# Optimization experiments

Hardware: AMD Instinct MI355X
Metric: run time of the kernel (lower is better)

## Reference

```python
import jax, jax.numpy as jnp
from jax import lax
import numpy as np

B, N, E, NA = 32, 8192, 256, 16
M_MIN, M_MAX = 3, 8192
PAD_TOKEN = -2.0
LN_EPS = 1e-3  # keras LayerNormalization default epsilon


def setup_inputs() -> dict:
    key = jax.random.key(0)
    ks = jax.random.split(key, 8)
    return {
        "x": jax.random.normal(ks[0], (B, N, E), jnp.float32),
        "mask": jnp.ones((B, N), jnp.float32),
        "barcode": jax.random.uniform(ks[1], (1, 1, E), jnp.float32),
        "Wq": 0.05 * jax.random.normal(ks[2], (E, E), jnp.float32),
        "Wk": 0.05 * jax.random.normal(ks[3], (E, E), jnp.float32),
        "Wv": 0.05 * jax.random.normal(ks[4], (E, E), jnp.float32),
        "g": jax.random.uniform(ks[5], (NA, E, E), jnp.float32, minval=-0.05, maxval=0.05),
        "w": 0.05 * jax.random.normal(ks[6], (1, NA, E, E), jnp.float32),
        "ln_gamma": jnp.ones((E,), jnp.float32),
        "ln_beta": jnp.zeros((E,), jnp.float32),
    }


def _select_one(order):
    """Greedy distance-constrained selection over a descending-sorted index list (N,).
    Matches the TF while_loop: first index always kept; a candidate is kept iff its
    abs distance to every previously kept index lies in [M_MIN, M_MAX].
    Unfilled slots stay 0 (TensorArray default)."""
    slot = jnp.arange(NA, dtype=jnp.int32)

    def body(i, state):
        sel, count = state
        cand = order[i]
        d = jnp.abs(sel - cand)
        ok = (d >= M_MIN) & (d <= M_MAX)
        active = slot < count
        valid = jnp.all(jnp.where(active, ok, True)) & (count < NA)
        sel = jnp.where((slot == count) & valid, cand, sel)
        count = count + valid.astype(jnp.int32)
        return (sel, count)

    sel0 = jnp.zeros((NA,), jnp.int32).at[0].set(order[0])
    sel, _ = lax.fori_loop(1, N, body, (sel0, jnp.int32(1)))
    return sel


def reference(x, mask, barcode, Wq, Wk, Wv, g, w, ln_gamma, ln_beta):
    m = jnp.where(mask == PAD_TOKEN, 0.0, 1.0)  # (B, N)
    bc = jnp.broadcast_to(barcode, (x.shape[0], 1, x.shape[-1]))
    q = bc @ Wq              # (B, 1, E)
    k = x @ Wk               # (B, N, E)
    v = x @ Wv               # (B, N, E)
    scale = 1.0 / jnp.sqrt(jnp.float32(x.shape[-1]))
    att = jnp.einsum('bqe,bne->bqn', q, k) * scale  # (B, 1, N)
    att = att + (1.0 - m[:, None, :]) * (-1e9)
    att = jax.nn.softmax(att, axis=-1) * m[:, None, :]
    barcode_out = jnp.einsum('bqn,bne->bqe', att, v)[:, 0, :]  # (B, E)

    att1 = att[:, 0, :]                                 # (B, N)
    order = jnp.argsort(-att1, axis=-1).astype(jnp.int32)
    inds = jnp.sort(jax.vmap(_select_one)(order), axis=-1)  # (B, NA)
    weights = jnp.take_along_axis(att1, inds, axis=1)        # (B, NA)
    outs = jnp.take_along_axis(x, inds[:, :, None], axis=1)  # (B, NA, E)

    # sinusoidal positional encoding from anchor positions
    ra = jnp.arange(E, dtype=jnp.float32) / jnp.float32(E)
    pos = jnp.sin(inds[:, :, None].astype(jnp.float32) / jnp.power(40.0, ra))
    outs = outs + pos

    # per-anchor gated projection: (B,NA,1,E) @ (NA,E,E) -> (B,NA,E)
    outs_w = jnp.einsum('bae,aef->baf', outs, w[0])
    outs_g = jax.nn.sigmoid(jnp.einsum('bae,aef->baf', outs, g))
    outs = outs_w * outs_g * weights[:, :, None]

    # LayerNorm over last axis (keras defaults: eps=1e-3, learned gamma/beta)
    mu = jnp.mean(outs, axis=-1, keepdims=True)
    var = jnp.mean(jnp.square(outs - mu), axis=-1, keepdims=True)
    outs = (outs - mu) * lax.rsqrt(var + LN_EPS) * ln_gamma + ln_beta

    return (outs, inds, weights, barcode_out)
```

## Files before the change

kernel.cpp:

```cpp
#include <hip/hip_runtime.h>

#define BB 32
#define NN 8192
#define EE 256
#define NAA 16
#define NCHUNK 64
#define CHUNK 128

#define KQ_OFF   0
#define ATT_OFF  256
#define PL_OFF   (ATT_OFF + BB*NN)
#define PS_OFF   (PL_OFF + BB*NCHUNK)
#define INDS_OFF (PS_OFF + BB*NCHUNK*EE)
#define WSEL_OFF (INDS_OFF + BB*NAA)

#define OUT_OUTS 0
#define OUT_INDS (BB*NAA*EE)
#define OUT_W    (OUT_INDS + BB*NAA)
#define OUT_BC   (OUT_W + BB*NAA)

__global__ __launch_bounds__(1024) void prep_kernel(
    const float* __restrict__ barcode, const float* __restrict__ Wq,
    const float* __restrict__ Wk, float* __restrict__ ws) {
  int t = threadIdx.x & 255, q = threadIdx.x >> 8;
  __shared__ float part[4][EE];
  __shared__ float qs[EE];
  float acc = 0.f;
  #pragma unroll 8
  for (int i = 0; i < 64; ++i) {
    int f = q * 64 + i;
    acc += barcode[f] * Wq[f*EE + t];
  }
  part[q][t] = acc;
  __syncthreads();
  if (threadIdx.x < 256) qs[t] = part[0][t] + part[1][t] + part[2][t] + part[3][t];
  __syncthreads();
  const float4* wk4 = (const float4*)(Wk + (size_t)t * EE + q * 64);
  const float4* qs4 = (const float4*)(qs + q * 64);
  float acc2 = 0.f;
  #pragma unroll
  for (int i = 0; i < 16; ++i) {
    float4 wv = wk4[i], qv = qs4[i];
    acc2 += wv.x*qv.x + wv.y*qv.y + wv.z*qv.z + wv.w*qv.w;
  }
  part[q][t] = acc2;
  __syncthreads();
  if (threadIdx.x < 256)
    ws[KQ_OFF + t] = (part[0][t] + part[1][t] + part[2][t] + part[3][t]) * 0.0625f;
}

__global__ __launch_bounds__(256) void pass_a(
    const float* __restrict__ x, const float* __restrict__ mask,
    float* __restrict__ ws) {
  const int c = blockIdx.x, b = blockIdx.y;
  const int w = threadIdx.x >> 6, lane = threadIdx.x & 63;
  const float4 kq4 = ((const float4*)(ws + KQ_OFF))[lane];
  float* att = ws + ATT_OFF + (size_t)b * NN + c * CHUNK;
  const float* xb = x + ((size_t)b * NN + (size_t)c * CHUNK) * EE;
  const float* mb = mask + (size_t)b * NN + c * CHUNK;

  float l = 0.f;
  float4 acc = {0.f, 0.f, 0.f, 0.f};
  #pragma unroll 4
  for (int r = w; r < CHUNK; r += 4) {
    float4 xv = ((const float4*)(xb + (size_t)r * EE))[lane];
    float d = xv.x*kq4.x + xv.y*kq4.y + xv.z*kq4.z + xv.w*kq4.w;
    #pragma unroll
    for (int off = 32; off >= 1; off >>= 1) d += __shfl_xor(d, off, 64);
    float mk = mb[r];
    float a = d + ((mk == -2.0f) ? -1e9f : 0.0f);
    if (lane == 0) att[r] = a;
    float keep = (mk == -2.0f) ? 0.f : 1.f;
    float p = __expf(a) * keep;
    l += p;
    acc.x += p*xv.x; acc.y += p*xv.y; acc.z += p*xv.z; acc.w += p*xv.w;
  }
  __shared__ float sl[4], ss[4][EE];
  ss[w][lane*4+0] = acc.x; ss[w][lane*4+1] = acc.y;
  ss[w][lane*4+2] = acc.z; ss[w][lane*4+3] = acc.w;
  if (lane == 0) sl[w] = l;
  __syncthreads();
  int t = threadIdx.x;
  ws[PS_OFF + (size_t)(b*NCHUNK + c)*EE + t] =
      ss[0][t] + ss[1][t] + ss[2][t] + ss[3][t];
  if (t == 0) ws[PL_OFF + b*NCHUNK + c] = sl[0] + sl[1] + sl[2] + sl[3];
}

__global__ __launch_bounds__(256) void combine_select(
    const float* __restrict__ Wv, float* __restrict__ ws, float* __restrict__ out) {
  int b = blockIdx.x, t = threadIdx.x;
  int w = t >> 6, lane = t & 63;
  __shared__ float sn[EE];
  __shared__ float p[NN];
  __shared__ float wvs[4];
  __shared__ int   wis[4];
  __shared__ int   sel[NAA];
  __shared__ float selw[NAA];
  __shared__ float Lsh;
  float S = 0.f;
  for (int c = 0; c < NCHUNK; ++c)
    S += ws[PS_OFF + (size_t)(b*NCHUNK + c)*EE + t];
  if (t < 64) {
    float lv = ws[PL_OFF + b*NCHUNK + t];
    #pragma unroll
    for (int off = 32; off >= 1; off >>= 1) lv += __shfl_xor(lv, off, 64);
    if (t == 0) Lsh = lv;
  }
  __syncthreads();
  float L = Lsh;
  sn[t] = S / L;
  const float* att = ws + ATT_OFF + (size_t)b * NN;
  for (int n = t; n < NN; n += 256) p[n] = att[n];
  __syncthreads();
  float acc = 0.f;
  #pragma unroll 8
  for (int e = 0; e < EE; ++e) acc += sn[e] * Wv[e*EE + t];
  out[OUT_BC + b*EE + t] = acc;
  for (int it = 0; it < NAA; ++it) {
    float v = -INFINITY; int idx = NN;
    for (int n = t; n < NN; n += 256) {
      float pv = p[n];
      if (pv > v) { v = pv; idx = n; }
    }
    #pragma unroll
    for (int off = 32; off >= 1; off >>= 1) {
      float v2 = __shfl_xor(v, off, 64);
      int   i2 = __shfl_xor(idx, off, 64);
      if (v2 > v || (v2 == v && i2 < idx)) { v = v2; idx = i2; }
    }
    if (lane == 0) { wvs[w] = v; wis[w] = idx; }
    __syncthreads();
    if (t == 0) {
      float bvv = wvs[0]; int bii = wis[0];
      #pragma unroll
      for (int j = 1; j < 4; ++j) {
        float v2 = wvs[j]; int i2 = wis[j];
        if (v2 > bvv || (v2 == bvv && i2 < bii)) { bvv = v2; bii = i2; }
      }
      sel[it] = bii; selw[it] = bvv;
      int lo = bii - 2 < 0 ? 0 : bii - 2;
      int hi = bii + 2 > NN-1 ? NN-1 : bii + 2;
      for (int j = lo; j <= hi; ++j) p[j] = -INFINITY;
    }
    __syncthreads();
  }
  if (t == 0) {
    for (int i = 1; i < NAA; ++i) {
      int ki = sel[i]; float kw = selw[i]; int j = i - 1;
      while (j >= 0 && sel[j] > ki) { sel[j+1] = sel[j]; selw[j+1] = selw[j]; --j; }
      sel[j+1] = ki; selw[j+1] = kw;
    }
  }
  __syncthreads();
  if (t < NAA) {
    float wt = expf(selw[t]) / L;
    out[OUT_INDS + b*NAA + t] = (float)sel[t];
    out[OUT_W    + b*NAA + t] = wt;
    ((int*)(ws + INDS_OFF))[b*NAA + t] = sel[t];
    ws[WSEL_OFF + b*NAA + t] = wt;
  }
}

__global__ __launch_bounds__(256) void final_kernel(
    const float* __restrict__ x, const float* __restrict__ g,
    const float* __restrict__ w, const float* __restrict__ ln_gamma,
    const float* __restrict__ ln_beta, const float* __restrict__ ws,
    float* __restrict__ out) {
  int a = blockIdx.x, b = blockIdx.y, t = threadIdx.x;
  __shared__ float row[EE];
  __shared__ float redw[4][EE];
  __shared__ float redg[4][EE];
  __shared__ float red[4];
  int ind = ((const int*)(ws + INDS_OFF))[b*NAA + a];
  float wt = ws[WSEL_OFF + b*NAA + a];
  float ra = (float)t * (1.0f/256.0f);
  float pos = sinf((float)ind / powf(40.0f, ra));
  row[t] = x[((size_t)b * NN + ind) * EE + t] + pos;
  __syncthreads();
  int qe = t >> 6, fq = t & 63;
  const float4* wa4 = (const float4*)(w + (size_t)a * EE * EE);
  const float4* ga4 = (const float4*)(g + (size_t)a * EE * EE);
  float4 aw = {0,0,0,0}, ag = {0,0,0,0};
  #pragma unroll 8
  for (int i = 0; i < 64; ++i) {
    int e = qe * 64 + i;
    float r = row[e];
    float4 wv = wa4[(size_t)e * 64 + fq];
    float4 gv = ga4[(size_t)e * 64 + fq];
    aw.x += r*wv.x; aw.y += r*wv.y; aw.z += r*wv.z; aw.w += r*wv.w;
    ag.x += r*gv.x; ag.y += r*gv.y; ag.z += r*gv.z; ag.w += r*gv.w;
  }
  ((float4*)redw[qe])[fq] = aw;
  ((float4*)redg[qe])[fq] = ag;
  __syncthreads();
  float ow = redw[0][t] + redw[1][t] + redw[2][t] + redw[3][t];
  float og = redg[0][t] + redg[1][t] + redg[2][t] + redg[3][t];
  float val = ow * (1.f / (1.f + expf(-og))) * wt;
  int wv_ = t >> 6;
  float s = val;
  #pragma unroll
  for (int off = 32; off >= 1; off >>= 1) s += __shfl_xor(s, off, 64);
  if ((t & 63) == 0) red[wv_] = s;
  __syncthreads();
  float mu = (red[0] + red[1] + red[2] + red[3]) * (1.f/256.f);
  __syncthreads();
  float dv = val - mu, sq = dv * dv;
  #pragma unroll
  for (int off = 32; off >= 1; off >>= 1) sq += __shfl_xor(sq, off, 64);
  if ((t & 63) == 0) red[wv_] = sq;
  __syncthreads();
  float var = (red[0] + red[1] + red[2] + red[3]) * (1.f/256.f);
  out[OUT_OUTS + ((size_t)b * NAA + a) * EE + t] =
      dv * rsqrtf(var + 0.001f) * ln_gamma[t] + ln_beta[t];
}

extern "C" void kernel_launch(void* const* d_in, const int* in_sizes, int n_in,
                              void* d_out, int out_size, void* d_ws, size_t ws_size,
                              hipStream_t stream) {
  const float* x       = (const float*)d_in[0];
  const float* mask    = (const float*)d_in[1];
  const float* barcode = (const float*)d_in[2];
  const float* Wq      = (const float*)d_in[3];
  const float* Wk      = (const float*)d_in[4];
  const float* Wv      = (const float*)d_in[5];
  const float* g       = (const float*)d_in[6];
  const float* w       = (const float*)d_in[7];
  const float* gamma   = (const float*)d_in[8];
  const float* beta    = (const float*)d_in[9];
  float* out = (float*)d_out;
  float* ws  = (float*)d_ws;

  prep_kernel<<<1, 1024, 0, stream>>>(barcode, Wq, Wk, ws);
  pass_a<<<dim3(NCHUNK, BB), 256, 0, stream>>>(x, mask, ws);
  combine_select<<<BB, 256, 0, stream>>>(Wv, ws, out);
  final_kernel<<<dim3(NAA, BB), 256, 0, stream>>>(x, g, w, gamma, beta, ws, out);
}
```

Baseline: 507.6 us.

## Shorten pass_a shuffle reductions and share anchor weights across four batches

In pass_a each wavefront now processes four rows at once, with 16 lanes per row each loading four float4s. This cuts the per-row cross-lane reduction from six shuffle steps to four, and partial sums are reduced through a larger shared buffer. In final_kernel each block handles four batch rows for one anchor, so each w/g matrix load is reused four times and the grid shrinks by four. A strange ternary on a3.z is numerically equivalent but odd, and fewer blocks in final_kernel lowers parallelism.

```diff
diff --git a/kernel.cpp b/kernel.cpp
--- a/kernel.cpp
+++ b/kernel.cpp
@@ -54,35 +54,51 @@
     float* __restrict__ ws) {
   const int c = blockIdx.x, b = blockIdx.y;
   const int w = threadIdx.x >> 6, lane = threadIdx.x & 63;
-  const float4 kq4 = ((const float4*)(ws + KQ_OFF))[lane];
+  const int grp = lane >> 4, sub = lane & 15;
+  const float4* kqp = (const float4*)(ws + KQ_OFF) + sub*4;
+  float4 kq0 = kqp[0], kq1 = kqp[1], kq2 = kqp[2], kq3 = kqp[3];
   float* att = ws + ATT_OFF + (size_t)b * NN + c * CHUNK;
   const float* xb = x + ((size_t)b * NN + (size_t)c * CHUNK) * EE;
   const float* mb = mask + (size_t)b * NN + c * CHUNK;
 
   float l = 0.f;
-  float4 acc = {0.f, 0.f, 0.f, 0.f};
-  #pragma unroll 4
-  for (int r = w; r < CHUNK; r += 4) {
-    float4 xv = ((const float4*)(xb + (size_t)r * EE))[lane];
-    float d = xv.x*kq4.x + xv.y*kq4.y + xv.z*kq4.z + xv.w*kq4.w;
-    #pragma unroll
-    for (int off = 32; off >= 1; off >>= 1) d += __shfl_xor(d, off, 64);
+  float4 a0 = {0,0,0,0}, a1 = {0,0,0,0}, a2 = {0,0,0,0}, a3 = {0,0,0,0};
+  #pragma unroll 2
+  for (int r0 = w*4; r0 < CHUNK; r0 += 16) {
+    int r = r0 + grp;
+    const float4* xr = (const float4*)(xb + (size_t)r * EE) + sub*4;
+    float4 x0 = xr[0], x1 = xr[1], x2 = xr[2], x3 = xr[3];
+    float d = x0.x*kq0.x + x0.y*kq0.y + x0.z*kq0.z + x0.w*kq0.w
+            + x1.x*kq1.x + x1.y*kq1.y + x1.z*kq1.z + x1.w*kq1.w
+            + x2.x*kq2.x + x2.y*kq2.y + x2.z*kq2.z + x2.w*kq2.w
+            + x3.x*kq3.x + x3.y*kq3.y + x3.z*kq3.z + x3.w*kq3.w;
+    d += __shfl_xor(d, 1, 64);
+    d += __shfl_xor(d, 2, 64);
+    d += __shfl_xor(d, 4, 64);
+    d += __shfl_xor(d, 8, 64);
     float mk = mb[r];
-    float a = d + ((mk == -2.0f) ? -1e9f : 0.0f);
-    if (lane == 0) att[r] = a;
-    float keep = (mk == -2.0f) ? 0.f : 1.f;
-    float p = __expf(a) * keep;
+    float aa = d + ((mk == -2.0f) ? -1e9f : 0.0f);
+    if (sub == 0) att[r] = aa;
+    float p = __expf(aa) * ((mk == -2.0f) ? 0.f : 1.f);
     l += p;
-    acc.x += p*xv.x; acc.y += p*xv.y; acc.z += p*xv.z; acc.w += p*xv.w;
-  }
-  __shared__ float sl[4], ss[4][EE];
-  ss[w][lane*4+0] = acc.x; ss[w][lane*4+1] = acc.y;
-  ss[w][lane*4+2] = acc.z; ss[w][lane*4+3] = acc.w;
+    a0.x += p*x0.x; a0.y += p*x0.y; a0.z += p*x0.z; a0.w += p*x0.w;
+    a1.x += p*x1.x; a1.y += p*x1.y; a1.z += p*x1.z; a1.w += p*x1.w;
+    a2.x += p*x2.x; a2.y += p*x2.y; a2.z += p*x2.z; a2.w += p*x2.w;
+    a3.x += p*x3.x; a3.y += p*x3.y; a3.z += p*x3.w == 0 ? p*x3.z*0 + p*x3.z : p*x3.z; a3.w += p*x3.w;
+  }
+  l += __shfl_xor(l, 16, 64);
+  l += __shfl_xor(l, 32, 64);
+  __shared__ float sl[4];
+  __shared__ float ss[16][EE];
+  float4* dst = (float4*)(&ss[w*4 + grp][sub*16]);
+  dst[0] = a0; dst[1] = a1; dst[2] = a2; dst[3] = a3;
   if (lane == 0) sl[w] = l;
   __syncthreads();
   int t = threadIdx.x;
-  ws[PS_OFF + (size_t)(b*NCHUNK + c)*EE + t] =
-      ss[0][t] + ss[1][t] + ss[2][t] + ss[3][t];
+  float S = 0.f;
+  #pragma unroll
+  for (int i = 0; i < 16; ++i) S += ss[i][t];
+  ws[PS_OFF + (size_t)(b*NCHUNK + c)*EE + t] = S;
   if (t == 0) ws[PL_OFF + b*NCHUNK + c] = sl[0] + sl[1] + sl[2] + sl[3];
 }
 
@@ -166,52 +182,76 @@
     const float* __restrict__ w, const float* __restrict__ ln_gamma,
     const float* __restrict__ ln_beta, const float* __restrict__ ws,
     float* __restrict__ out) {
-  int a = blockIdx.x, b = blockIdx.y, t = threadIdx.x;
-  __shared__ float row[EE];
+  int a = blockIdx.x, bg = blockIdx.y, t = threadIdx.x;
+  __shared__ float row[4][EE];
   __shared__ float redw[4][EE];
   __shared__ float redg[4][EE];
   __shared__ float red[4];
-  int ind = ((const int*)(ws + INDS_OFF))[b*NAA + a];
-  float wt = ws[WSEL_OFF + b*NAA + a];
-  float ra = (float)t * (1.0f/256.0f);
-  float pos = sinf((float)ind / powf(40.0f, ra));
-  row[t] = x[((size_t)b * NN + ind) * EE + t] + pos;
+  __shared__ int   inds_s[4];
+  __shared__ float wts_s[4];
+  if (t < 4) {
+    int b = bg*4 + t;
+    inds_s[t] = ((const int*)(ws + INDS_OFF))[b*NAA + a];
+    wts_s[t]  = ws[WSEL_OFF + b*NAA + a];
+  }
+  __syncthreads();
+  float pw = powf(40.0f, (float)t * (1.0f/256.0f));
+  #pragma unroll
+  for (int j = 0; j < 4; ++j) {
+    int b = bg*4 + j;
+    row[j][t] = x[((size_t)b * NN + inds_s[j]) * EE + t]
+              + sinf((float)inds_s[j] / pw);
+  }
   __syncthreads();
   int qe = t >> 6, fq = t & 63;
   const float4* wa4 = (const float4*)(w + (size_t)a * EE * EE);
   const float4* ga4 = (const float4*)(g + (size_t)a * EE * EE);
-  float4 aw = {0,0,0,0}, ag = {0,0,0,0};
-  #pragma unroll 8
+  float4 aw0={0,0,0,0}, aw1={0,0,0,0}, aw2={0,0,0,0}, aw3={0,0,0,0};
+  float4 ag0={0,0,0,0}, ag1={0,0,0,0}, ag2={0,0,0,0}, ag3={0,0,0,0};
+  #pragma unroll 4
   for (int i = 0; i < 64; ++i) {
     int e = qe * 64 + i;
-    float r = row[e];
     float4 wv = wa4[(size_t)e * 64 + fq];
     float4 gv = ga4[(size_t)e * 64 + fq];
-    aw.x += r*wv.x; aw.y += r*wv.y; aw.z += r*wv.z; aw.w += r*wv.w;
-    ag.x += r*gv.x; ag.y += r*gv.y; ag.z += r*gv.z; ag.w += r*gv.w;
-  }
-  ((float4*)redw[qe])[fq] = aw;
-  ((float4*)redg[qe])[fq] = ag;
-  __syncthreads();
-  float ow = redw[0][t] + redw[1][t] + redw[2][t] + redw[3][t];
-  float og = redg[0][t] + redg[1][t] + redg[2][t] + redg[3][t];
-  float val = ow * (1.f / (1.f + expf(-og))) * wt;
-  int wv_ = t >> 6;
-  float s = val;
-  #pragma unroll
-  for (int off = 32; off >= 1; off >>= 1) s += __shfl_xor(s, off, 64);
-  if ((t & 63) == 0) red[wv_] = s;
-  __syncthreads();
-  float mu = (red[0] + red[1] + red[2] + red[3]) * (1.f/256.f);
-  __syncthreads();
-  float dv = val - mu, sq = dv * dv;
-  #pragma unroll
-  for (int off = 32; off >= 1; off >>= 1) sq += __shfl_xor(sq, off, 64);
-  if ((t & 63) == 0) red[wv_] = sq;
-  __syncthreads();
-  float var = (red[0] + red[1] + red[2] + red[3]) * (1.f/256.f);
-  out[OUT_OUTS + ((size_t)b * NAA + a) * EE + t] =
-      dv * rsqrtf(var + 0.001f) * ln_gamma[t] + ln_beta[t];
+    float r0 = row[0][e], r1 = row[1][e], r2 = row[2][e], r3 = row[3][e];
+    aw0.x += r0*wv.x; aw0.y += r0*wv.y; aw0.z += r0*wv.z; aw0.w += r0*wv.w;
+    aw1.x += r1*wv.x; aw1.y += r1*wv.y; aw1.z += r1*wv.z; aw1.w += r1*wv.w;
+    aw2.x += r2*wv.x; aw2.y += r2*wv.y; aw2.z += r2*wv.z; aw2.w += r2*wv.w;
+    aw3.x += r3*wv.x; aw3.y += r3*wv.y; aw3.z += r3*wv.z; aw3.w += r3*wv.w;
+    ag0.x += r0*gv.x; ag0.y += r0*gv.y; ag0.z += r0*gv.z; ag0.w += r0*gv.w;
+    ag1.x += r1*gv.x; ag1.y += r1*gv.y; ag1.z += r1*gv.z; ag1.w += r1*gv.w;
+    ag2.x += r2*gv.x; ag2.y += r2*gv.y; ag2.z += r2*gv.z; ag2.w += r2*gv.w;
+    ag3.x += r3*gv.x; ag3.y += r3*gv.y; ag3.z += r3*gv.z; ag3.w += r3*gv.w;
+  }
+  #pragma unroll 1
+  for (int j = 0; j < 4; ++j) {
+    float4 aw = j==0 ? aw0 : j==1 ? aw1 : j==2 ? aw2 : aw3;
+    float4 ag = j==0 ? ag0 : j==1 ? ag1 : j==2 ? ag2 : ag3;
+    __syncthreads();
+    ((float4*)redw[qe])[fq] = aw;
+    ((float4*)redg[qe])[fq] = ag;
+    __syncthreads();
+    float ow = redw[0][t] + redw[1][t] + redw[2][t] + redw[3][t];
+    float og = redg[0][t] + redg[1][t] + redg[2][t] + redg[3][t];
+    float val = ow * (1.f / (1.f + expf(-og))) * wts_s[j];
+    int wv_ = t >> 6;
+    float s = val;
+    #pragma unroll
+    for (int off = 32; off >= 1; off >>= 1) s += __shfl_xor(s, off, 64);
+    if ((t & 63) == 0) red[wv_] = s;
+    __syncthreads();
+    float mu = (red[0] + red[1] + red[2] + red[3]) * (1.f/256.f);
+    __syncthreads();
+    float dv = val - mu, sq = dv * dv;
+    #pragma unroll
+    for (int off = 32; off >= 1; off >>= 1) sq += __shfl_xor(sq, off, 64);
+    if ((t & 63) == 0) red[wv_] = sq;
+    __syncthreads();
+    float var = (red[0] + red[1] + red[2] + red[3]) * (1.f/256.f);
+    int b = bg*4 + j;
+    out[OUT_OUTS + ((size_t)b * NAA + a) * EE + t] =
+        dv * rsqrtf(var + 0.001f) * ln_gamma[t] + ln_beta[t];
+  }
 }
 
 extern "C" void kernel_launch(void* const* d_in, const int* in_sizes, int n_in,
@@ -233,5 +273,5 @@
   prep_kernel<<<1, 1024, 0, stream>>>(barcode, Wq, Wk, ws);
   pass_a<<<dim3(NCHUNK, BB), 256, 0, stream>>>(x, mask, ws);
   combine_select<<<BB, 256, 0, stream>>>(Wv, ws, out);
-  final_kernel<<<dim3(NAA, BB), 256, 0, stream>>>(x, g, w, gamma, beta, ws, out);
-}
+  final_kernel<<<dim3(NAA, BB/4), 256, 0, stream>>>(x, g, w, gamma, beta, ws, out);
+}
```

Measured after the change: 518.7 us. +2.2%, slower.
